# Kernel tuning notes

Measured on AMD Instinct MI355X. Metric: run time of the kernel, lower is better.

The kernel has to match this reference:

```python
import jax, jax.numpy as jnp
import numpy as np

B, C, IN, H = 64, 128, 1024, 512  # batch, channels, input features (=='seq_length' arg), hidden


def setup_inputs() -> dict:
    key = jax.random.key(0)
    ks = jax.random.split(key, 9)
    s = 1.0 / np.sqrt(H)  # PyTorch LSTM init: U(-1/sqrt(H), 1/sqrt(H))
    u = lambda k, shape: jax.random.uniform(k, shape, jnp.float32, -s, s)
    return {
        "x": jax.random.normal(ks[0], (B, C, IN), jnp.float32),
        # layer 0: one weight set per direction (fwd, bwd)
        "W_ih0": u(ks[1], (2, 4 * H, IN)),
        "W_hh0": u(ks[2], (2, 4 * H, H)),
        "b_ih0": u(ks[3], (2, 4 * H)),
        "b_hh0": u(ks[4], (2, 4 * H)),
        # layers 1..2: input is concat of both directions (2H)
        "W_ih12": u(ks[5], (2, 2, 4 * H, 2 * H)),
        "W_hh12": u(ks[6], (2, 2, 4 * H, H)),
        "b_ih12": u(ks[7], (2, 2, 4 * H)),
        "b_hh12": u(ks[8], (2, 2, 4 * H)),
    }


def _cell(inp, W_ih, b_ih, b_hh):
    # One LSTM step from zero state (h0 = c0 = 0): W_hh @ h0 == 0, f*c0 == 0.
    gates = inp @ W_ih.T + b_ih + b_hh  # [N, 4H]
    i, f, g, o = jnp.split(gates, 4, axis=-1)  # PyTorch gate order: i, f, g, o
    c = jax.nn.sigmoid(i) * jnp.tanh(g)
    return jax.nn.sigmoid(o) * jnp.tanh(c)  # h, shape [N, H]


def reference(x, W_ih0, W_hh0, b_ih0, b_hh0, W_ih12, W_hh12, b_ih12, b_hh12):
    b, c, n = x.shape
    # Each channel is an independent seq-len-1 LSTM call with zero init state,
    # so fold channels into the batch dimension. W_hh* contribute nothing (h0=0).
    xb = x.reshape(b * c, n)
    h = jnp.concatenate(
        [_cell(xb, W_ih0[d], b_ih0[d], b_hh0[d]) for d in range(2)], axis=-1
    )  # [b*c, 2H]
    for l in range(2):  # layers 1 and 2
        h = jnp.concatenate(
            [_cell(h, W_ih12[l, d], b_ih12[l, d], b_hh12[l, d]) for d in range(2)],
            axis=-1,
        )
    return h.reshape(b, c, 2 * H)  # [batch, channels, 2*hidden]
```

## Files before the change

### kernel.cpp

```cpp
#include <hip/hip_runtime.h>


typedef float f32x4 __attribute__((ext_vector_type(4)));
typedef short short8 __attribute__((ext_vector_type(8)));
typedef unsigned short u16;

#define NP 3072
#define MROWS 8192
#define KDIM 1024

__device__ __forceinline__ u16 f2bf(float f) {
  unsigned u = __float_as_uint(f);
  u += 0x7fffu + ((u >> 16) & 1u);
  return (u16)(u >> 16);
}

__device__ __forceinline__ float sigmoid_f(float x) {
  return 1.0f / (1.0f + __expf(-x));
}
__device__ __forceinline__ float tanh_f(float x) {
  float xc = fminf(fmaxf(x, -15.0f), 15.0f);
  float e = __expf(2.0f * xc);
  return (e - 1.0f) / (e + 1.0f);
}

__device__ __forceinline__ void gload_lds16(const void* g, void* l) {
  __builtin_amdgcn_global_load_lds((const __attribute__((address_space(1))) void*)g,
                                   (__attribute__((address_space(3))) void*)l,
                                   16, 0, 0);
}


__global__ __launch_bounds__(256) void k_convert_x(const float* __restrict__ x,
                                                   u16* __restrict__ out) {
  int tid = blockIdx.x * 256 + threadIdx.x;
  const float4* src = (const float4*)x + (size_t)tid * 2;
  float4 v0 = src[0], v1 = src[1];
  union { u16 u[8]; uint4 v; } r;
  r.u[0] = f2bf(v0.x); r.u[1] = f2bf(v0.y); r.u[2] = f2bf(v0.z); r.u[3] = f2bf(v0.w);
  r.u[4] = f2bf(v1.x); r.u[5] = f2bf(v1.y); r.u[6] = f2bf(v1.z); r.u[7] = f2bf(v1.w);
  ((uint4*)out)[tid] = r.v;
}

__global__ __launch_bounds__(256) void k_pack_w(const float* __restrict__ Wih0,
                                                const float* __restrict__ Wih12,
                                                u16* __restrict__ P) {
  int tid = blockIdx.x * 256 + threadIdx.x;
  int s   = tid / (NP * 128);
  int rem = tid - s * (NP * 128);
  int p   = rem >> 7;
  int k8  = rem & 127;
  int hb = p / 48;
  int pr = p - hb * 48;
  int gs = pr >> 4;
  int hl = pr & 15;
  int hcol = hb * 16 + hl;
  int dir = hcol >> 9;
  int h   = hcol & 511;
  int og  = (gs == 0) ? 0 : (gs + 1);
  const float* src;
  if (s == 0)
    src = Wih0 + ((size_t)(dir * 2048 + og * 512 + h)) * 1024 + k8 * 8;
  else
    src = Wih12 + ((size_t)(((s - 1) * 2 + dir) * 2048 + og * 512 + h)) * 1024 + k8 * 8;
  float4 v0 = ((const float4*)src)[0];
  float4 v1 = ((const float4*)src)[1];
  union { u16 u[8]; uint4 v; } r;
  r.u[0] = f2bf(v0.x); r.u[1] = f2bf(v0.y); r.u[2] = f2bf(v0.z); r.u[3] = f2bf(v0.w);
  r.u[4] = f2bf(v1.x); r.u[5] = f2bf(v1.y); r.u[6] = f2bf(v1.z); r.u[7] = f2bf(v1.w);
  ((uint4*)P)[tid] = r.v;
}

__global__ __launch_bounds__(256) void k_pack_bias(const float* __restrict__ bih0,
                                                   const float* __restrict__ bhh0,
                                                   const float* __restrict__ bih12,
                                                   const float* __restrict__ bhh12,
                                                   float* __restrict__ pb) {
  int tid = blockIdx.x * 256 + threadIdx.x;
  if (tid >= 3 * NP) return;
  int s = tid / NP;
  int p = tid - s * NP;
  int hb = p / 48;
  int pr = p - hb * 48;
  int gs = pr >> 4;
  int hl = pr & 15;
  int hcol = hb * 16 + hl;
  int dir = hcol >> 9;
  int h   = hcol & 511;
  int og  = (gs == 0) ? 0 : (gs + 1);
  int j   = og * 512 + h;
  float v;
  if (s == 0) {
    int i = dir * 2048 + j;
    v = bih0[i] + bhh0[i];
  } else {
    int i = ((s - 1) * 2 + dir) * 2048 + j;
    v = bih12[i] + bhh12[i];
  }
  pb[tid] = v;
}

template <bool F32OUT>
__global__ __launch_bounds__(256) void k_lstm_gemm(const u16* __restrict__ A,
                                                   const u16* __restrict__ Bp,
                                                   const float* __restrict__ bias,
                                                   void* __restrict__ outp) {
  __shared__ uint4 lds[2][1280];
  const int t    = threadIdx.x;
  const int lane = t & 63;
  const int w    = t >> 6;
  const int wr   = w >> 1, wc = w & 1;
  const int r16  = lane & 15, kg = lane >> 4;
  const int brow = blockIdx.y * 128;
  const int bn0  = blockIdx.x * 192;

  f32x4 acc[4][6];
#pragma unroll
  for (int m = 0; m < 4; ++m)
#pragma unroll
    for (int n = 0; n < 6; ++n) acc[m][n] = (f32x4){0.f, 0.f, 0.f, 0.f};

  auto stage = [&](int buf, int kt) {
    char* base = (char*)lds[buf];
#pragma unroll
    for (int it = 0; it < 2; ++it) {
      int j = t + it * 256;
      int rr = j >> 2, k16 = j & 3;
      const u16* src = A + (size_t)(brow + rr) * KDIM + kt * 32 + ((k16 ^ ((rr >> 1) & 3)) << 3);
      gload_lds16(src, base + j * 16);
    }
#pragma unroll
    for (int it = 0; it < 3; ++it) {
      int jb = t + it * 256;
      int rr = jb >> 2, k16 = jb & 3;
      const u16* src = Bp + (size_t)(bn0 + rr) * KDIM + kt * 32 + ((k16 ^ ((rr >> 1) & 3)) << 3);
      gload_lds16(src, base + 8192 + jb * 16);
    }
  };

  stage(0, 0);
  __syncthreads();

  int cur = 0;
  const int sw = (r16 >> 1) & 3;
  for (int kt = 0; kt < 32; ++kt) {
    if (kt < 31) stage(cur ^ 1, kt + 1);
    const char* Ab = (const char*)lds[cur];
    const char* Bb = Ab + 8192;
    short8 a[4], b[6];
#pragma unroll
    for (int m = 0; m < 4; ++m) {
      int row = wr * 64 + m * 16 + r16;
      a[m] = *(const short8*)(Ab + row * 64 + ((kg ^ sw) << 4));
    }
#pragma unroll
    for (int n = 0; n < 6; ++n) {
      int pr = wc * 96 + n * 16 + r16;
      b[n] = *(const short8*)(Bb + pr * 64 + ((kg ^ sw) << 4));
    }
#pragma unroll
    for (int m = 0; m < 4; ++m)
#pragma unroll
      for (int n = 0; n < 6; ++n)
        acc[m][n] = __builtin_amdgcn_mfma_f32_16x16x32_bf16(a[m], b[n], acc[m][n], 0, 0, 0);
    __syncthreads();
    cur ^= 1;
  }

#pragma unroll
  for (int hb2 = 0; hb2 < 2; ++hb2) {
    int pbase = bn0 + wc * 96 + hb2 * 48;
    float bi = bias[pbase + r16];
    float bg = bias[pbase + 16 + r16];
    float bo = bias[pbase + 32 + r16];
    int hcol = (pbase / 48) * 16 + r16;
#pragma unroll
    for (int m = 0; m < 4; ++m) {
      int rowb = brow + wr * 64 + m * 16 + kg * 4;
#pragma unroll
      for (int r = 0; r < 4; ++r) {
        float vi = acc[m][hb2 * 3 + 0][r] + bi;
        float vg = acc[m][hb2 * 3 + 1][r] + bg;
        float vo = acc[m][hb2 * 3 + 2][r] + bo;
        float c  = sigmoid_f(vi) * tanh_f(vg);
        float hv = sigmoid_f(vo) * tanh_f(c);
        size_t oidx = (size_t)(rowb + r) * 1024 + hcol;
        if (F32OUT) ((float*)outp)[oidx] = hv;
        else        ((u16*)outp)[oidx]   = f2bf(hv);
      }
    }
  }
}

extern "C" void kernel_launch(void* const* d_in, const int* in_sizes, int n_in,
                              void* d_out, int out_size, void* d_ws, size_t ws_size,
                              hipStream_t stream) {
  const float* x     = (const float*)d_in[0];
  const float* Wih0  = (const float*)d_in[1];
  const float* bih0  = (const float*)d_in[3];
  const float* bhh0  = (const float*)d_in[4];
  const float* Wih12 = (const float*)d_in[5];
  const float* bih12 = (const float*)d_in[7];
  const float* bhh12 = (const float*)d_in[8];

  char* ws = (char*)d_ws;
  u16*   xbf = (u16*)ws;
  u16*   h1  = (u16*)(ws + 16777216);
  u16*   h2  = (u16*)(ws + 33554432);
  u16*   P3  = (u16*)(ws + 50331648);
  float* pb3 = (float*)(ws + 69206016);

  k_convert_x<<<4096, 256, 0, stream>>>(x, xbf);
  k_pack_w<<<4608, 256, 0, stream>>>(Wih0, Wih12, P3);
  k_pack_bias<<<36, 256, 0, stream>>>(bih0, bhh0, bih12, bhh12, pb3);

  dim3 grid(NP / 192, MROWS / 128);
  k_lstm_gemm<false><<<grid, 256, 0, stream>>>(xbf, P3, pb3, h1);
  k_lstm_gemm<false><<<grid, 256, 0, stream>>>(h1, P3 + (size_t)NP * KDIM, pb3 + NP, h2);
  k_lstm_gemm<true ><<<grid, 256, 0, stream>>>(h2, P3 + (size_t)2 * NP * KDIM, pb3 + 2 * NP, d_out);
}
```

Baseline: 243.8 us.

## Rewrite LSTM GEMM as 8-wave 256x192x64 tile with phased MFMA/load pipeline

The fused LSTM GEMM kernel moves from a 128x192 tile with BK=32 and 4 waves to a 256x192 tile with BK=64 and 8 waves. Each wave's work is split into four phases that interleave LDS reads, async global-to-LDS staging of the next tile, and MFMA bursts. The phases use explicit barriers, vmcnt waits, sched_barrier and setprio. The goal is more data reuse per tile and better overlap of memory traffic with matrix math. In exchange it uses about 112KB of LDS per block, and correctness depends on the hand-placed waitcnt and barriers.

After: 203.3 us. 1.2x faster.

```diff
diff --git a/kernel.cpp b/kernel.cpp
--- a/kernel.cpp
+++ b/kernel.cpp
@@ -8,13 +8,18 @@
 #define NP 3072
 #define MROWS 8192
 #define KDIM 1024
+#define BM 256
+#define BN 192
+#define BK 64
+#define LDS_A_SZ (BM * BK * 2)
+#define LDS_B_SZ (BN * BK * 2)
+#define LDS_B_OFF (2 * LDS_A_SZ)
 
 __device__ __forceinline__ u16 f2bf(float f) {
   unsigned u = __float_as_uint(f);
   u += 0x7fffu + ((u >> 16) & 1u);
   return (u16)(u >> 16);
 }
-
 __device__ __forceinline__ float sigmoid_f(float x) {
   return 1.0f / (1.0f + __expf(-x));
 }
@@ -23,7 +28,6 @@
   float e = __expf(2.0f * xc);
   return (e - 1.0f) / (e + 1.0f);
 }
-
 __device__ __forceinline__ void gload_lds16(const void* g, void* l) {
   __builtin_amdgcn_global_load_lds((const __attribute__((address_space(1))) void*)g,
                                    (__attribute__((address_space(3))) void*)l,
@@ -100,88 +104,132 @@
   pb[tid] = v;
 }
 
+
+#define BAR()    __builtin_amdgcn_s_barrier()
+#define SCHEDB() __builtin_amdgcn_sched_barrier(0)
+#define WAITV(N) asm volatile("s_waitcnt vmcnt(" #N ")" ::: "memory")
+#define MM(Macc, Aop, Bop) Macc = __builtin_amdgcn_mfma_f32_16x16x32_bf16(Aop, Bop, Macc, 0, 0, 0)
+
+#define LDA(MQ, K32, M4, BUF) \
+  (*(const short8*)(lds + ((K32) ? aK1 : aK0) + ((BUF) * LDS_A_SZ + (MQ) * 8192 + (M4) * 2048)))
+#define LDB(N3, K32, BUF) \
+  (*(const short8*)(lds + ((K32) ? bK1 : bK0) + ((BUF) * LDS_B_SZ + (N3) * 2048)))
+
+#define STAGE_B(RB, BUF, KT) \
+  gload_lds16(srcB + (size_t)(RB) * 64 * KDIM + (size_t)(KT) * BK, \
+              lds + LDS_B_OFF + (BUF) * LDS_B_SZ + (RB) * 8192 + t * 16)
+#define STAGE_A(ROWB, BUF, KT) \
+  gload_lds16(srcA + (size_t)(ROWB) * KDIM + (size_t)(KT) * BK, \
+              lds + (BUF) * LDS_A_SZ + (ROWB) * 128 + t * 16)
+
+#define PH_READS_A(MQ, K32, BUF) \
+  a0 = LDA(MQ, K32, 0, BUF); a1 = LDA(MQ, K32, 1, BUF); \
+  a2 = LDA(MQ, K32, 2, BUF); a3 = LDA(MQ, K32, 3, BUF);
+
+#define PH_MFMA(MQ, B0_, B1_, B2_) \
+  __builtin_amdgcn_s_setprio(1); \
+  MM(acc[(MQ)*4+0][0], a0, B0_); MM(acc[(MQ)*4+1][0], a1, B0_); \
+  MM(acc[(MQ)*4+2][0], a2, B0_); MM(acc[(MQ)*4+3][0], a3, B0_); \
+  MM(acc[(MQ)*4+0][1], a0, B1_); MM(acc[(MQ)*4+1][1], a1, B1_); \
+  MM(acc[(MQ)*4+2][1], a2, B1_); MM(acc[(MQ)*4+3][1], a3, B1_); \
+  MM(acc[(MQ)*4+0][2], a0, B2_); MM(acc[(MQ)*4+1][2], a1, B2_); \
+  MM(acc[(MQ)*4+2][2], a2, B2_); MM(acc[(MQ)*4+3][2], a3, B2_); \
+  __builtin_amdgcn_s_setprio(0);
+
+#define TILE(BUF, KT, DO_STAGE, LASTMID) \
+  { \
+     \
+    PH_READS_A(0, 0, BUF); \
+    b00 = LDB(0, 0, BUF); b01 = LDB(1, 0, BUF); b02 = LDB(2, 0, BUF); \
+    if (DO_STAGE) { STAGE_B(0, (BUF)^1, (KT)+1); STAGE_B(1, (BUF)^1, (KT)+1); } \
+    BAR(); \
+    PH_MFMA(0, b00, b01, b02); \
+    BAR(); \
+     \
+    PH_READS_A(0, 1, BUF); \
+    b10 = LDB(0, 1, BUF); b11 = LDB(1, 1, BUF); b12 = LDB(2, 1, BUF); \
+    if (DO_STAGE) { STAGE_B(2, (BUF)^1, (KT)+1); STAGE_A(0, (BUF)^1, (KT)+1); } \
+    BAR(); \
+    PH_MFMA(0, b10, b11, b12); \
+    if (LASTMID) { WAITV(0); } else { WAITV(4); } \
+    BAR(); SCHEDB(); \
+     \
+    PH_READS_A(1, 0, BUF); \
+    if (DO_STAGE) { STAGE_A(128, (BUF)^1, (KT)+1); STAGE_A(64, (BUF)^1, (KT)+1); } \
+    BAR(); \
+    PH_MFMA(1, b00, b01, b02); \
+    BAR(); \
+     \
+    PH_READS_A(1, 1, BUF); \
+    if (DO_STAGE) { STAGE_A(192, (BUF)^1, (KT)+1); } \
+    BAR(); \
+    PH_MFMA(1, b10, b11, b12); \
+    if (DO_STAGE) { WAITV(2); } \
+    BAR(); SCHEDB(); \
+  }
+
 template <bool F32OUT>
-__global__ __launch_bounds__(256) void k_lstm_gemm(const u16* __restrict__ A,
-                                                   const u16* __restrict__ Bp,
-                                                   const float* __restrict__ bias,
-                                                   void* __restrict__ outp) {
-  __shared__ uint4 lds[2][1280];
+__global__ __launch_bounds__(512, 2) void k_lstm_gemm8(const u16* __restrict__ A,
+                                                       const u16* __restrict__ Bp,
+                                                       const float* __restrict__ bias,
+                                                       void* __restrict__ outp) {
+  __shared__ __align__(16) char lds[114688];
   const int t    = threadIdx.x;
   const int lane = t & 63;
   const int w    = t >> 6;
-  const int wr   = w >> 1, wc = w & 1;
+  const int wr   = w >> 2;
+  const int wc   = w & 3;
   const int r16  = lane & 15, kg = lane >> 4;
-  const int brow = blockIdx.y * 128;
-  const int bn0  = blockIdx.x * 192;
-
-  f32x4 acc[4][6];
-#pragma unroll
-  for (int m = 0; m < 4; ++m)
-#pragma unroll
-    for (int n = 0; n < 6; ++n) acc[m][n] = (f32x4){0.f, 0.f, 0.f, 0.f};
-
-  auto stage = [&](int buf, int kt) {
-    char* base = (char*)lds[buf];
-#pragma unroll
-    for (int it = 0; it < 2; ++it) {
-      int j = t + it * 256;
-      int rr = j >> 2, k16 = j & 3;
-      const u16* src = A + (size_t)(brow + rr) * KDIM + kt * 32 + ((k16 ^ ((rr >> 1) & 3)) << 3);
-      gload_lds16(src, base + j * 16);
-    }
-#pragma unroll
-    for (int it = 0; it < 3; ++it) {
-      int jb = t + it * 256;
-      int rr = jb >> 2, k16 = jb & 3;
-      const u16* src = Bp + (size_t)(bn0 + rr) * KDIM + kt * 32 + ((k16 ^ ((rr >> 1) & 3)) << 3);
-      gload_lds16(src, base + 8192 + jb * 16);
-    }
-  };
-
-  stage(0, 0);
-  __syncthreads();
-
-  int cur = 0;
-  const int sw = (r16 >> 1) & 3;
-  for (int kt = 0; kt < 32; ++kt) {
-    if (kt < 31) stage(cur ^ 1, kt + 1);
-    const char* Ab = (const char*)lds[cur];
-    const char* Bb = Ab + 8192;
-    short8 a[4], b[6];
-#pragma unroll
-    for (int m = 0; m < 4; ++m) {
-      int row = wr * 64 + m * 16 + r16;
-      a[m] = *(const short8*)(Ab + row * 64 + ((kg ^ sw) << 4));
-    }
-#pragma unroll
-    for (int n = 0; n < 6; ++n) {
-      int pr = wc * 96 + n * 16 + r16;
-      b[n] = *(const short8*)(Bb + pr * 64 + ((kg ^ sw) << 4));
-    }
-#pragma unroll
-    for (int m = 0; m < 4; ++m)
-#pragma unroll
-      for (int n = 0; n < 6; ++n)
-        acc[m][n] = __builtin_amdgcn_mfma_f32_16x16x32_bf16(a[m], b[n], acc[m][n], 0, 0, 0);
-    __syncthreads();
-    cur ^= 1;
-  }
-
-#pragma unroll
-  for (int hb2 = 0; hb2 < 2; ++hb2) {
-    int pbase = bn0 + wc * 96 + hb2 * 48;
-    float bi = bias[pbase + r16];
-    float bg = bias[pbase + 16 + r16];
-    float bo = bias[pbase + 32 + r16];
-    int hcol = (pbase / 48) * 16 + r16;
-#pragma unroll
-    for (int m = 0; m < 4; ++m) {
-      int rowb = brow + wr * 64 + m * 16 + kg * 4;
+  const int brow = blockIdx.y * BM;
+  const int bn0  = blockIdx.x * BN;
+
+  const int sw    = r16 & 7;
+  const int slot0 = kg ^ sw;
+  const int aK0 = wr * 16384 + r16 * 128 + slot0 * 16;
+  const int aK1 = wr * 16384 + r16 * 128 + (slot0 ^ 4) * 16;
+  const int bK0 = LDS_B_OFF + (wc * 48 + r16) * 128 + slot0 * 16;
+  const int bK1 = LDS_B_OFF + (wc * 48 + r16) * 128 + (slot0 ^ 4) * 16;
+
+  const int rr   = t >> 3;
+  const int koct = ((t & 7) ^ (rr & 7)) << 3;
+  const u16* srcA = A  + (size_t)(brow + rr) * KDIM + koct;
+  const u16* srcB = Bp + (size_t)(bn0  + rr) * KDIM + koct;
+
+  f32x4 acc[8][3];
+#pragma unroll
+  for (int m = 0; m < 8; ++m)
+#pragma unroll
+    for (int n = 0; n < 3; ++n) acc[m][n] = (f32x4){0.f, 0.f, 0.f, 0.f};
+
+  short8 a0, a1, a2, a3, b00, b01, b02, b10, b11, b12;
+
+  STAGE_B(0, 0, 0); STAGE_B(1, 0, 0); STAGE_B(2, 0, 0);
+  STAGE_A(0, 0, 0); STAGE_A(128, 0, 0); STAGE_A(64, 0, 0); STAGE_A(192, 0, 0);
+  WAITV(2);
+  BAR(); SCHEDB();
+
+  for (int k2 = 0; k2 < 7; ++k2) {
+    int kt = k2 * 2;
+    TILE(0, kt, 1, 0);
+    TILE(1, kt + 1, 1, 0);
+  }
+  TILE(0, 14, 1, 0);
+  TILE(1, 15, 0, 1);
+
+  {
+    int pb = bn0 + wc * 48;
+    float biV = bias[pb + r16];
+    float bgV = bias[pb + 16 + r16];
+    float boV = bias[pb + 32 + r16];
+    int hcol = (blockIdx.x * 4 + wc) * 16 + r16;
+#pragma unroll
+    for (int m8 = 0; m8 < 8; ++m8) {
+      int rowb = brow + wr * 128 + (m8 >> 2) * 64 + (m8 & 3) * 16 + kg * 4;
 #pragma unroll
       for (int r = 0; r < 4; ++r) {
-        float vi = acc[m][hb2 * 3 + 0][r] + bi;
-        float vg = acc[m][hb2 * 3 + 1][r] + bg;
-        float vo = acc[m][hb2 * 3 + 2][r] + bo;
+        float vi = acc[m8][0][r] + biV;
+        float vg = acc[m8][1][r] + bgV;
+        float vo = acc[m8][2][r] + boV;
         float c  = sigmoid_f(vi) * tanh_f(vg);
         float hv = sigmoid_f(vo) * tanh_f(c);
         size_t oidx = (size_t)(rowb + r) * 1024 + hcol;
@@ -214,8 +262,8 @@
   k_pack_w<<<4608, 256, 0, stream>>>(Wih0, Wih12, P3);
   k_pack_bias<<<36, 256, 0, stream>>>(bih0, bhh0, bih12, bhh12, pb3);
 
-  dim3 grid(NP / 192, MROWS / 128);
-  k_lstm_gemm<false><<<grid, 256, 0, stream>>>(xbf, P3, pb3, h1);
-  k_lstm_gemm<false><<<grid, 256, 0, stream>>>(h1, P3 + (size_t)NP * KDIM, pb3 + NP, h2);
-  k_lstm_gemm<true ><<<grid, 256, 0, stream>>>(h2, P3 + (size_t)2 * NP * KDIM, pb3 + 2 * NP, d_out);
-}
+  dim3 grid(NP / BN, MROWS / BM);
+  k_lstm_gemm8<false><<<grid, 512, 0, stream>>>(xbf, P3, pb3, h1);
+  k_lstm_gemm8<false><<<grid, 512, 0, stream>>>(h1, P3 + (size_t)NP * KDIM, pb3 + NP, h2);
+  k_lstm_gemm8<true ><<<grid, 512, 0, stream>>>(h2, P3 + (size_t)2 * NP * KDIM, pb3 + 2 * NP, d_out);
+}
```

## Shrink GEMM tile to 128x96, remap blocks for L2 locality, unroll K loop

Applied to the files above, without the earlier changes.

The fused LSTM GEMM tile drops from 128x192 to 128x96, which halves accumulator registers and raises the occupancy target to 4 blocks per CU. The grid doubles to 2048 blocks. Block indices are remapped into 8 chunks of 16x16 tiles to improve L2 reuse of A and B. The K loop is manually unrolled with precomputed LDS offsets. The smaller tile lowers arithmetic intensity per block and increases total global and LDS traffic.

Measured after the change: 233.0 us. 4.4% less time.

```diff
diff --git a/kernel.cpp b/kernel.cpp
--- a/kernel.cpp
+++ b/kernel.cpp
@@ -8,13 +8,16 @@
 #define NP 3072
 #define MROWS 8192
 #define KDIM 1024
+#define BM 128
+#define BN 96
+#define BK 32
+#define LDS_TILE 14336
 
 __device__ __forceinline__ u16 f2bf(float f) {
   unsigned u = __float_as_uint(f);
   u += 0x7fffu + ((u >> 16) & 1u);
   return (u16)(u >> 16);
 }
-
 __device__ __forceinline__ float sigmoid_f(float x) {
   return 1.0f / (1.0f + __expf(-x));
 }
@@ -23,7 +26,6 @@
   float e = __expf(2.0f * xc);
   return (e - 1.0f) / (e + 1.0f);
 }
-
 __device__ __forceinline__ void gload_lds16(const void* g, void* l) {
   __builtin_amdgcn_global_load_lds((const __attribute__((address_space(1))) void*)g,
                                    (__attribute__((address_space(3))) void*)l,
@@ -100,90 +102,95 @@
   pb[tid] = v;
 }
 
+
+#define MM(Macc, Aop, Bop) Macc = __builtin_amdgcn_mfma_f32_16x16x32_bf16(Aop, Bop, Macc, 0, 0, 0)
+
+#define STAGE(BUF, KT) \
+  gload_lds16(srcA + (size_t)(KT) * BK,              lds + (BUF) * LDS_TILE + t * 16); \
+  gload_lds16(srcA + 64 * KDIM + (size_t)(KT) * BK,  lds + (BUF) * LDS_TILE + 4096 + t * 16); \
+  gload_lds16(srcB + (size_t)(KT) * BK,              lds + (BUF) * LDS_TILE + 8192 + t * 16); \
+  if (t < 128) { gload_lds16(srcB + 64 * KDIM + (size_t)(KT) * BK, lds + (BUF) * LDS_TILE + 12288 + t * 16); }
+
+#define KSTEP(BUF, KT, DOST) \
+  { \
+    if (DOST) { STAGE((BUF)^1, (KT)+1); } \
+    const char* base = lds + (BUF) * LDS_TILE; \
+    short8 a0 = *(const short8*)(base + aOff); \
+    short8 a1 = *(const short8*)(base + aOff + 1024); \
+    short8 a2 = *(const short8*)(base + aOff + 2048); \
+    short8 a3 = *(const short8*)(base + aOff + 3072); \
+    short8 b0 = *(const short8*)(base + bOff); \
+    short8 b1 = *(const short8*)(base + bOff + 1024); \
+    short8 b2 = *(const short8*)(base + bOff + 2048); \
+    MM(acc[0][0], a0, b0); MM(acc[1][0], a1, b0); MM(acc[2][0], a2, b0); MM(acc[3][0], a3, b0); \
+    MM(acc[0][1], a0, b1); MM(acc[1][1], a1, b1); MM(acc[2][1], a2, b1); MM(acc[3][1], a3, b1); \
+    MM(acc[0][2], a0, b2); MM(acc[1][2], a1, b2); MM(acc[2][2], a2, b2); MM(acc[3][2], a3, b2); \
+    __syncthreads(); \
+  }
+
 template <bool F32OUT>
-__global__ __launch_bounds__(256) void k_lstm_gemm(const u16* __restrict__ A,
-                                                   const u16* __restrict__ Bp,
-                                                   const float* __restrict__ bias,
-                                                   void* __restrict__ outp) {
-  __shared__ uint4 lds[2][1280];
+__global__ __launch_bounds__(256, 4) void k_lstm_gemm97(const u16* __restrict__ A,
+                                                        const u16* __restrict__ Bp,
+                                                        const float* __restrict__ bias,
+                                                        void* __restrict__ outp) {
+  __shared__ __align__(16) char lds[2 * LDS_TILE];
   const int t    = threadIdx.x;
   const int lane = t & 63;
   const int w    = t >> 6;
-  const int wr   = w >> 1, wc = w & 1;
+  const int wr   = w >> 1;
+  const int wc   = w & 1;
   const int r16  = lane & 15, kg = lane >> 4;
-  const int brow = blockIdx.y * 128;
-  const int bn0  = blockIdx.x * 192;
-
-  f32x4 acc[4][6];
+
+  const int n_hw = blockIdx.y * gridDim.x + blockIdx.x;
+  const int c    = n_hw & 7;
+  const int wlc  = n_hw >> 3;
+  const int bx   = (c & 1) * 16 + (wlc & 15);
+  const int by   = (c >> 1) * 16 + (wlc >> 4);
+  const int brow = by * BM;
+  const int bn0  = bx * BN;
+
+  const int sw   = (r16 >> 1) & 3;
+  const int slot = (kg ^ sw) << 4;
+  const int aOff = wr * 4096 + r16 * 64 + slot;
+  const int bOff = 8192 + wc * 3072 + r16 * 64 + slot;
+
+  const int srow = t >> 2;
+  const int koct = ((t & 3) ^ ((t >> 3) & 3)) << 3;
+  const u16* srcA = A  + (size_t)(brow + srow) * KDIM + koct;
+  const u16* srcB = Bp + (size_t)(bn0  + srow) * KDIM + koct;
+
+  f32x4 acc[4][3];
 #pragma unroll
   for (int m = 0; m < 4; ++m)
 #pragma unroll
-    for (int n = 0; n < 6; ++n) acc[m][n] = (f32x4){0.f, 0.f, 0.f, 0.f};
-
-  auto stage = [&](int buf, int kt) {
-    char* base = (char*)lds[buf];
-#pragma unroll
-    for (int it = 0; it < 2; ++it) {
-      int j = t + it * 256;
-      int rr = j >> 2, k16 = j & 3;
-      const u16* src = A + (size_t)(brow + rr) * KDIM + kt * 32 + ((k16 ^ ((rr >> 1) & 3)) << 3);
-      gload_lds16(src, base + j * 16);
-    }
-#pragma unroll
-    for (int it = 0; it < 3; ++it) {
-      int jb = t + it * 256;
-      int rr = jb >> 2, k16 = jb & 3;
-      const u16* src = Bp + (size_t)(bn0 + rr) * KDIM + kt * 32 + ((k16 ^ ((rr >> 1) & 3)) << 3);
-      gload_lds16(src, base + 8192 + jb * 16);
-    }
-  };
-
-  stage(0, 0);
+    for (int n = 0; n < 3; ++n) acc[m][n] = (f32x4){0.f, 0.f, 0.f, 0.f};
+
+  STAGE(0, 0);
   __syncthreads();
 
-  int cur = 0;
-  const int sw = (r16 >> 1) & 3;
-  for (int kt = 0; kt < 32; ++kt) {
-    if (kt < 31) stage(cur ^ 1, kt + 1);
-    const char* Ab = (const char*)lds[cur];
-    const char* Bb = Ab + 8192;
-    short8 a[4], b[6];
-#pragma unroll
-    for (int m = 0; m < 4; ++m) {
-      int row = wr * 64 + m * 16 + r16;
-      a[m] = *(const short8*)(Ab + row * 64 + ((kg ^ sw) << 4));
-    }
-#pragma unroll
-    for (int n = 0; n < 6; ++n) {
-      int pr = wc * 96 + n * 16 + r16;
-      b[n] = *(const short8*)(Bb + pr * 64 + ((kg ^ sw) << 4));
-    }
-#pragma unroll
-    for (int m = 0; m < 4; ++m)
-#pragma unroll
-      for (int n = 0; n < 6; ++n)
-        acc[m][n] = __builtin_amdgcn_mfma_f32_16x16x32_bf16(a[m], b[n], acc[m][n], 0, 0, 0);
-    __syncthreads();
-    cur ^= 1;
-  }
-
-#pragma unroll
-  for (int hb2 = 0; hb2 < 2; ++hb2) {
-    int pbase = bn0 + wc * 96 + hb2 * 48;
-    float bi = bias[pbase + r16];
-    float bg = bias[pbase + 16 + r16];
-    float bo = bias[pbase + 32 + r16];
-    int hcol = (pbase / 48) * 16 + r16;
+  for (int k2 = 0; k2 < 15; ++k2) {
+    KSTEP(0, 2 * k2, 1);
+    KSTEP(1, 2 * k2 + 1, 1);
+  }
+  KSTEP(0, 30, 1);
+  KSTEP(1, 31, 0);
+
+  {
+    int pbase = bn0 + wc * 48;
+    float biV = bias[pbase + r16];
+    float bgV = bias[pbase + 16 + r16];
+    float boV = bias[pbase + 32 + r16];
+    int hcol = (2 * bx + wc) * 16 + r16;
 #pragma unroll
     for (int m = 0; m < 4; ++m) {
       int rowb = brow + wr * 64 + m * 16 + kg * 4;
 #pragma unroll
       for (int r = 0; r < 4; ++r) {
-        float vi = acc[m][hb2 * 3 + 0][r] + bi;
-        float vg = acc[m][hb2 * 3 + 1][r] + bg;
-        float vo = acc[m][hb2 * 3 + 2][r] + bo;
-        float c  = sigmoid_f(vi) * tanh_f(vg);
-        float hv = sigmoid_f(vo) * tanh_f(c);
+        float vi = acc[m][0][r] + biV;
+        float vg = acc[m][1][r] + bgV;
+        float vo = acc[m][2][r] + boV;
+        float c2 = sigmoid_f(vi) * tanh_f(vg);
+        float hv = sigmoid_f(vo) * tanh_f(c2);
         size_t oidx = (size_t)(rowb + r) * 1024 + hcol;
         if (F32OUT) ((float*)outp)[oidx] = hv;
         else        ((u16*)outp)[oidx]   = f2bf(hv);
@@ -214,8 +221,8 @@
   k_pack_w<<<4608, 256, 0, stream>>>(Wih0, Wih12, P3);
   k_pack_bias<<<36, 256, 0, stream>>>(bih0, bhh0, bih12, bhh12, pb3);
 
-  dim3 grid(NP / 192, MROWS / 128);
-  k_lstm_gemm<false><<<grid, 256, 0, stream>>>(xbf, P3, pb3, h1);
-  k_lstm_gemm<false><<<grid, 256, 0, stream>>>(h1, P3 + (size_t)NP * KDIM, pb3 + NP, h2);
-  k_lstm_gemm<true ><<<grid, 256, 0, stream>>>(h2, P3 + (size_t)2 * NP * KDIM, pb3 + 2 * NP, d_out);
-}
+  dim3 grid(NP / BN, MROWS / BM);
+  k_lstm_gemm97<false><<<grid, 256, 0, stream>>>(xbf, P3, pb3, h1);
+  k_lstm_gemm97<false><<<grid, 256, 0, stream>>>(h1, P3 + (size_t)NP * KDIM, pb3 + NP, h2);
+  k_lstm_gemm97<true ><<<grid, 256, 0, stream>>>(h2, P3 + (size_t)2 * NP * KDIM, pb3 + 2 * NP, d_out);
+}
```
